# Performance work log

Measured on AMD Instinct MI355X. Metric: run time of the kernel, lower is better.

Reference implementation:

```python
import jax, jax.numpy as jnp
import numpy as np

B, N, C, K, OUT = 2, 8192, 64, 20, 64
EDGE_DIM = C * 3 + 5  # 197
BN_EPS = 1e-5


def setup_inputs() -> dict:
    key = jax.random.key(0)
    k1, k2 = jax.random.split(key, 2)
    x = jax.random.normal(k1, (B, C, N), jnp.float32)
    conv_w = jax.random.normal(k2, (OUT, EDGE_DIM), jnp.float32) * 0.05
    return {
        "x": x,
        "conv_w": conv_w,
        "bn_gamma": jnp.ones((OUT,), jnp.float32),
        "bn_beta": jnp.zeros((OUT,), jnp.float32),
        "bn_mean": jnp.zeros((OUT,), jnp.float32),
        "bn_var": jnp.ones((OUT,), jnp.float32),
        "k": K,
    }


def reference(x, conv_w, bn_gamma, bn_beta, bn_mean, bn_var, k):
    xt = jnp.transpose(x, (0, 2, 1))          # [B, N, C]
    b, n, c = xt.shape
    xyz = xt[:, :, :3]                         # [B, N, 3]

    # ---- kNN on xyz (negative squared distance, top-k) ----
    inner = -2.0 * jnp.matmul(xyz, jnp.transpose(xyz, (0, 2, 1)))  # [B,N,N]
    xx = jnp.sum(xyz * xyz, axis=2, keepdims=True)                 # [B,N,1]
    pd = -xx - inner - jnp.transpose(xx, (0, 2, 1))                # [B,N,N]
    _, idx = jax.lax.top_k(pd, k)                                  # [B,N,k]

    # ---- gather neighbors ----
    neighbors = jax.vmap(lambda xi, ii: xi[ii])(xt, idx)           # [B,N,k,C]
    x_ctr = xt[:, :, None, :]                                      # [B,N,1,C]
    base = jnp.concatenate(
        [jnp.broadcast_to(x_ctr, (b, n, k, c)), neighbors - x_ctr, neighbors],
        axis=3)                                                    # [B,N,k,3C]

    # ---- geometric features ----
    xyz_nb = neighbors[:, :, :, :3]
    vec = xyz_nb - xyz[:, :, None, :]                              # [B,N,k,3]
    dist = jnp.linalg.norm(vec, axis=3, keepdims=True)             # [B,N,k,1]
    local_density = jnp.broadcast_to(dist.mean(axis=2, keepdims=True), dist.shape)
    z_ctr = xyz[:, :, 2:3]                                         # [B,N,1]
    z_nb = xyz_nb[:, :, :, 2:3]                                    # [B,N,k,1]
    rel_h = jnp.broadcast_to(z_ctr[:, :, None, :] - z_nb.mean(axis=2, keepdims=True), dist.shape)
    dist_var = jnp.broadcast_to(jnp.var(dist, axis=2, keepdims=True, ddof=1), dist.shape)
    vn = vec / (dist + 1e-6)
    md = vn.mean(axis=2, keepdims=True)
    md = md / (jnp.linalg.norm(md, axis=3, keepdims=True) + 1e-6)
    cos = jnp.sum(vn * md, axis=3, keepdims=True)
    angle = 1.0 - jnp.abs(cos)

    edge = jnp.concatenate([base, dist, local_density, rel_h, dist_var, angle], axis=3)  # [B,N,k,EDGE_DIM]

    # ---- 1x1 conv + BN (inference stats) + LeakyReLU(0.2) + max over neighbors ----
    y = jnp.einsum('bnkf,of->bnko', edge, conv_w)                  # [B,N,k,OUT]
    scale = bn_gamma / jnp.sqrt(bn_var + BN_EPS)
    y = (y - bn_mean) * scale + bn_beta
    y = jnp.where(y >= 0, y, 0.2 * y)
    out = y.max(axis=2)                                            # [B,N,OUT]
    return jnp.transpose(out, (0, 2, 1))                           # [B,OUT,N]
```

## Files before the change

kernel.cpp:

```cpp
#include <hip/hip_runtime.h>


#define NPTS 8192
#define NBATCH 2
#define NQ (NBATCH * NPTS)
#define CH 64
#define KNN 20
#define EDIM 197
#define QW 4
#define KWAVES 16
#define QB (QW * KWAVES)
#define CAPC 64

__device__ __forceinline__ float wsum(float v) {
  v += __shfl_xor(v, 1, 64);
  v += __shfl_xor(v, 2, 64);
  v += __shfl_xor(v, 4, 64);
  v += __shfl_xor(v, 8, 64);
  v += __shfl_xor(v, 16, 64);
  v += __shfl_xor(v, 32, 64);
  return v;
}

__device__ __forceinline__ float dtilde(float m2x, float m2y, float m2z, float4 c) {
  return fmaf(m2x, c.x, fmaf(m2y, c.y, fmaf(m2z, c.z, c.w)));
}

__device__ __forceinline__ double d2d(float qx, float qy, float qz, float4 c) {
  double dx = (double)qx - (double)c.x;
  double dy = (double)qy - (double)c.y;
  double dz = (double)qz - (double)c.z;
  return dx * dx + dy * dy + dz * dz;
}

__device__ __forceinline__ float bcastf(float v, int l) {
  return __int_as_float(__builtin_amdgcn_readlane(__float_as_int(v), l));
}

__global__ __launch_bounds__(256) void proj_kernel(const float* __restrict__ x,
                                                   const float* __restrict__ w,
                                                   float4* __restrict__ cpack,
                                                   float* __restrict__ projc,
                                                   float* __restrict__ projn) {
  __shared__ float wl[CH * 16];
  int by = blockIdx.y;
  int mat = by >> 2, oq = by & 3;
  for (int i = threadIdx.x; i < CH * 16; i += 256) {
    int c = i >> 4, oo = i & 15;
    int o = oq * 16 + oo;
    float w1 = w[o * EDIM + c];
    float w2 = w[o * EDIM + 64 + c];
    float w3 = w[o * EDIM + 128 + c];
    wl[i] = mat ? (w2 + w3) : (w1 - w2);
  }
  __syncthreads();
  int p = blockIdx.x * 256 + threadIdx.x;
  int b = p >> 13, n = p & (NPTS - 1);
  const float* xb = x + (size_t)b * CH * NPTS + n;
  float acc[16];
#pragma unroll
  for (int o = 0; o < 16; ++o) acc[o] = 0.f;
#pragma unroll 4
  for (int c = 0; c < CH; ++c) {
    float xv = xb[(size_t)c * NPTS];
    const float4* wr = (const float4*)(wl + c * 16);
#pragma unroll
    for (int o4 = 0; o4 < 4; ++o4) {
      float4 wv = wr[o4];
      acc[o4 * 4 + 0] = fmaf(wv.x, xv, acc[o4 * 4 + 0]);
      acc[o4 * 4 + 1] = fmaf(wv.y, xv, acc[o4 * 4 + 1]);
      acc[o4 * 4 + 2] = fmaf(wv.z, xv, acc[o4 * 4 + 2]);
      acc[o4 * 4 + 3] = fmaf(wv.w, xv, acc[o4 * 4 + 3]);
    }
  }
  float* dst = (mat ? projn : projc) + (size_t)p * 64 + oq * 16;
#pragma unroll
  for (int o4 = 0; o4 < 4; ++o4)
    ((float4*)dst)[o4] = make_float4(acc[o4 * 4 + 0], acc[o4 * 4 + 1],
                                     acc[o4 * 4 + 2], acc[o4 * 4 + 3]);
  if (by == 0) {
    float cx = xb[0], cy = xb[(size_t)NPTS], cz = xb[(size_t)2 * NPTS];
    cpack[p] = make_float4(cx, cy, cz, fmaf(cx, cx, fmaf(cy, cy, cz * cz)));
  }
}

__global__ __launch_bounds__(1024) void knnfeat_kernel(const float4* __restrict__ cpack,
                                                       const float* __restrict__ projc,
                                                       const float* __restrict__ projn,
                                                       const float* __restrict__ w,
                                                       const float* __restrict__ gamma,
                                                       const float* __restrict__ beta,
                                                       const float* __restrict__ mean,
                                                       const float* __restrict__ var,
                                                       float* __restrict__ out) {
  __shared__ float4 t4[NPTS];
  __shared__ int lidx[KWAVES][QW][CAPC];
  __shared__ int nsel[KWAVES][QW][KNN];
  int tid = threadIdx.x;
  int lane = tid & 63;
  int wq = tid >> 6;
  int blk = blockIdx.x;
  int bb = blk >> 7;
  int q0 = blk * QB + wq * QW;
  const float4* cb = cpack + bb * NPTS;

  for (int i = tid; i < NPTS; i += 1024) t4[i] = cb[i];
  float qx[QW], qy[QW], qz[QW], m2x[QW], m2y[QW], m2z[QW];
#pragma unroll
  for (int qi = 0; qi < QW; ++qi) {
    float4 qp = cpack[q0 + qi];
    qx[qi] = qp.x; qy[qi] = qp.y; qz[qi] = qp.z;
    m2x[qi] = -2.f * qp.x; m2y[qi] = -2.f * qp.y; m2z[qi] = -2.f * qp.z;
  }
  __syncthreads();

  float m[QW];
#pragma unroll
  for (int qi = 0; qi < QW; ++qi) m[qi] = 3.0e38f;
#pragma unroll 2
  for (int i = 0; i < NPTS / 64; ++i) {
    float4 c = t4[lane + i * 64];
#pragma unroll
    for (int qi = 0; qi < QW; ++qi)
      m[qi] = fminf(m[qi], dtilde(m2x[qi], m2y[qi], m2z[qi], c));
  }
  float lo[QW], hi[QW];
#pragma unroll
  for (int qi = 0; qi < QW; ++qi) { lo[qi] = -256.f; hi[qi] = 256.f; }
#pragma unroll 1
  for (int it = 0; it < 24; ++it) {
#pragma unroll
    for (int qi = 0; qi < QW; ++qi) {
      float mid = (lo[qi] + hi[qi]) * 0.5f;
      int c = (int)__popcll(__ballot(m[qi] <= mid));
      if (c >= KNN) hi[qi] = mid; else lo[qi] = mid;
    }
  }

  int cnt[QW];
#pragma unroll
  for (int qi = 0; qi < QW; ++qi) cnt[qi] = 0;
  unsigned long long lmlt = (1ull << lane) - 1ull;
#pragma unroll 2
  for (int i = 0; i < NPTS / 64; ++i) {
    float4 c = t4[lane + i * 64];
#pragma unroll
    for (int qi = 0; qi < QW; ++qi) {
      bool pr = dtilde(m2x[qi], m2y[qi], m2z[qi], c) <= hi[qi];
      unsigned long long mk = __ballot(pr);
      if (mk) {
        int ofs = cnt[qi] + (int)__popcll(mk & lmlt);
        if (pr && ofs < CAPC) lidx[wq][qi][ofs] = lane + i * 64;
        cnt[qi] += (int)__popcll(mk);
      }
    }
  }

  double dd[QW]; int ii[QW]; int cC[QW];
#pragma unroll
  for (int qi = 0; qi < QW; ++qi) {
    cC[qi] = min(cnt[qi], CAPC);
    dd[qi] = 1e300; ii[qi] = -1;
    if (lane < cC[qi]) {
      int id = lidx[wq][qi][lane];
      dd[qi] = d2d(qx[qi], qy[qi], qz[qi], t4[id]);
      ii[qi] = id;
    }
  }
#pragma unroll
  for (int qi = 0; qi < QW; ++qi) {
    int xlo = __double2loint(dd[qi]), xhi = __double2hiint(dd[qi]);
    int r = 0;
#pragma unroll 1
    for (int j = 0; j < cC[qi]; ++j) {
      double dj = __hiloint2double(__builtin_amdgcn_readlane(xhi, j),
                                   __builtin_amdgcn_readlane(xlo, j));
      int idj = __builtin_amdgcn_readlane(ii[qi], j);
      r += (dj < dd[qi]) || (dj == dd[qi] && idj < ii[qi]);
    }
    if (ii[qi] >= 0 && r < KNN) nsel[wq][qi][r] = ii[qi];
  }

  float* zbuf = (float*)&lidx[0][0][0];
  float wd  = w[lane * EDIM + 192];
  float wld = w[lane * EDIM + 193];
  float wrh = w[lane * EDIM + 194];
  float wdv = w[lane * EDIM + 195];
  float wa  = w[lane * EDIM + 196];
  float sc = gamma[lane] / sqrtf(var[lane] + 1e-5f);
  float muv = mean[lane], bt = beta[lane];
#pragma unroll 2
  for (int qi = 0; qi < QW; ++qi) {
    int gq = q0 + qi;
    int jj = nsel[wq][qi][lane < KNN ? lane : 0] & (NPTS - 1);
    float4 nb = t4[jj];
    float vx = nb.x - qx[qi], vy = nb.y - qy[qi], vz = nb.z - qz[qi];
    float dist = sqrtf(fmaf(vx, vx, fmaf(vy, vy, vz * vz)));
    float inv = 1.f / (dist + 1e-6f);
    float vnx = vx * inv, vny = vy * inv, vnz = vz * inv;
    float msk = (lane < KNN) ? 1.f : 0.f;
    float sd = wsum(dist * msk);
    float szn = wsum(nb.z * msk);
    float sx = wsum(vnx * msk);
    float sy = wsum(vny * msk);
    float s3 = wsum(vnz * msk);
    float ld = sd * (1.f / KNN);
    float rh = qz[qi] - szn * (1.f / KNN);
    float dev = dist - ld;
    float dvs = wsum(dev * dev * msk);
    float dv = dvs * (1.f / (KNN - 1));
    float mdx = sx * (1.f / KNN), mdy = sy * (1.f / KNN), mdz = s3 * (1.f / KNN);
    float mnorm = sqrtf(fmaf(mdx, mdx, fmaf(mdy, mdy, mdz * mdz)));
    float rinv = 1.f / (mnorm + 1e-6f);
    mdx *= rinv; mdy *= rinv; mdz *= rinv;
    float cosv = vnx * mdx + vny * mdy + vnz * mdz;
    float angle = 1.f - fabsf(cosv);
    float base = projc[(size_t)gq * 64 + lane] + ld * wld + rh * wrh + dv * wdv;
    float zmax = -3.0e38f, zmin = 3.0e38f;
#pragma unroll
    for (int kk = 0; kk < KNN; ++kk) {
      float dk = bcastf(dist, kk);
      float ak = bcastf(angle, kk);
      int jk = __builtin_amdgcn_readlane(jj, kk);
      float z = base + projn[(size_t)(bb * NPTS + jk) * 64 + lane] + dk * wd + ak * wa;
      zmax = fmaxf(zmax, z);
      zmin = fminf(zmin, z);
    }
    float M = (sc >= 0.f) ? zmax : zmin;
    float yv = (M - muv) * sc + bt;
    yv = (yv >= 0.f) ? yv : 0.2f * yv;
    int qcol = wq * QW + qi;
    zbuf[qcol * 64 + ((lane + qcol) & 63)] = yv;
  }
  __syncthreads();
  {
    int o = tid >> 4, g = tid & 15;
    int n0 = (blk & 127) * 64;
    int q4 = g * 4;
    float4 v;
    v.x = zbuf[(q4 + 0) * 64 + ((o + q4 + 0) & 63)];
    v.y = zbuf[(q4 + 1) * 64 + ((o + q4 + 1) & 63)];
    v.z = zbuf[(q4 + 2) * 64 + ((o + q4 + 2) & 63)];
    v.w = zbuf[(q4 + 3) * 64 + ((o + q4 + 3) & 63)];
    *(float4*)(out + (size_t)bb * CH * NPTS + (size_t)o * NPTS + n0 + q4) = v;
  }
}

extern "C" void kernel_launch(void* const* d_in, const int* in_sizes, int n_in,
                              void* d_out, int out_size, void* d_ws, size_t ws_size,
                              hipStream_t stream) {
  const float* x = (const float*)d_in[0];
  const float* w = (const float*)d_in[1];
  const float* gamma = (const float*)d_in[2];
  const float* beta = (const float*)d_in[3];
  const float* mean = (const float*)d_in[4];
  const float* var = (const float*)d_in[5];
  float* out = (float*)d_out;

  const size_t OFF_CPACK = 0;
  const size_t OFF_PROJC = 262144;
  const size_t OFF_PROJN = 262144 + 4194304;
  const size_t NEED = 262144 + 8388608;
  if (ws_size < NEED) return;

  char* ws = (char*)d_ws;
  float4* cpack = (float4*)(ws + OFF_CPACK);
  float* projc = (float*)(ws + OFF_PROJC);
  float* projn = (float*)(ws + OFF_PROJN);

  proj_kernel<<<dim3(64, 8), 256, 0, stream>>>(x, w, cpack, projc, projn);
  knnfeat_kernel<<<256, 1024, 0, stream>>>(cpack, projc, projn, w,
                                           gamma, beta, mean, var, out);
}
```

Measured before the change: 79.46 us.

## Replace brute-force kNN scan with z-bucket sorted spatial search

```diff
diff --git a/kernel.cpp b/kernel.cpp
--- a/kernel.cpp
+++ b/kernel.cpp
@@ -3,14 +3,19 @@
 
 #define NPTS 8192
 #define NBATCH 2
-#define NQ (NBATCH * NPTS)
 #define CH 64
 #define KNN 20
 #define EDIM 197
-#define QW 4
+#define NBUCK 1024
+#define CAPC 128
 #define KWAVES 16
-#define QB (QW * KWAVES)
-#define CAPC 64
+#define QW 2
+#define QB (KWAVES * QW)
+
+__device__ __forceinline__ int zbucket(float z) {
+  int b = (int)((z + 4.5f) * (1024.0f / 9.0f));
+  return b < 0 ? 0 : (b > 1023 ? 1023 : b);
+}
 
 __device__ __forceinline__ float wsum(float v) {
   v += __shfl_xor(v, 1, 64);
@@ -37,11 +42,17 @@
   return __int_as_float(__builtin_amdgcn_readlane(__float_as_int(v), l));
 }
 
+__global__ __launch_bounds__(1024) void zeroh_kernel(int* __restrict__ hist) {
+  int t = blockIdx.x * 1024 + threadIdx.x;
+  if (t < NBATCH * NBUCK) hist[t] = 0;
+}
+
 __global__ __launch_bounds__(256) void proj_kernel(const float* __restrict__ x,
                                                    const float* __restrict__ w,
                                                    float4* __restrict__ cpack,
                                                    float* __restrict__ projc,
-                                                   float* __restrict__ projn) {
+                                                   float* __restrict__ projn,
+                                                   int* __restrict__ hist) {
   __shared__ float wl[CH * 16];
   int by = blockIdx.y;
   int mat = by >> 2, oq = by & 3;
@@ -81,122 +92,187 @@
   if (by == 0) {
     float cx = xb[0], cy = xb[(size_t)NPTS], cz = xb[(size_t)2 * NPTS];
     cpack[p] = make_float4(cx, cy, cz, fmaf(cx, cx, fmaf(cy, cy, cz * cz)));
-  }
-}
-
-__global__ __launch_bounds__(1024) void knnfeat_kernel(const float4* __restrict__ cpack,
-                                                       const float* __restrict__ projc,
-                                                       const float* __restrict__ projn,
-                                                       const float* __restrict__ w,
-                                                       const float* __restrict__ gamma,
-                                                       const float* __restrict__ beta,
-                                                       const float* __restrict__ mean,
-                                                       const float* __restrict__ var,
-                                                       float* __restrict__ out) {
-  __shared__ float4 t4[NPTS];
-  __shared__ int lidx[KWAVES][QW][CAPC];
-  __shared__ int nsel[KWAVES][QW][KNN];
+    atomicAdd(&hist[b * NBUCK + zbucket(cz)], 1);
+  }
+}
+
+__global__ __launch_bounds__(1024) void prefix_kernel(const int* __restrict__ hist,
+                                                      int* __restrict__ off,
+                                                      int* __restrict__ cursor) {
+  __shared__ int s[NBUCK];
   int tid = threadIdx.x;
-  int lane = tid & 63;
-  int wq = tid >> 6;
+  for (int b = 0; b < NBATCH; ++b) {
+    s[tid] = hist[b * NBUCK + tid];
+    __syncthreads();
+    for (int o = 1; o < NBUCK; o <<= 1) {
+      int t = (tid >= o) ? s[tid - o] : 0;
+      __syncthreads();
+      s[tid] += t;
+      __syncthreads();
+    }
+    int excl = tid ? s[tid - 1] : 0;
+    off[b * (NBUCK + 1) + tid] = excl;
+    cursor[b * NBUCK + tid] = excl;
+    if (tid == NBUCK - 1) off[b * (NBUCK + 1) + NBUCK] = s[NBUCK - 1];
+    __syncthreads();
+  }
+}
+
+__global__ __launch_bounds__(256) void scatter_kernel(const float4* __restrict__ cpack,
+                                                      int* __restrict__ cursor,
+                                                      float4* __restrict__ s4g,
+                                                      int* __restrict__ sidxg) {
+  int t = blockIdx.x * 256 + threadIdx.x;
+  int b = t >> 13, n = t & (NPTS - 1);
+  float4 c = cpack[t];
+  int slot = atomicAdd(&cursor[b * NBUCK + zbucket(c.z)], 1);
+  s4g[b * NPTS + slot] = c;
+  sidxg[b * NPTS + slot] = n;
+}
+
+__global__ __launch_bounds__(1024, 8) void knnfeat_kernel(const float4* __restrict__ cpack,
+                                                          const float4* __restrict__ s4g,
+                                                          const int* __restrict__ sidxg,
+                                                          const int* __restrict__ off,
+                                                          const float* __restrict__ projc,
+                                                          const float* __restrict__ projn,
+                                                          const float* __restrict__ w,
+                                                          const float* __restrict__ gamma,
+                                                          const float* __restrict__ beta,
+                                                          const float* __restrict__ mean,
+                                                          const float* __restrict__ var,
+                                                          float* __restrict__ out) {
+  __shared__ int offL[NBUCK + 1];
+  __shared__ unsigned short lidx[KWAVES][CAPC];
+  __shared__ int nselL[KWAVES][KNN];
+  __shared__ float zbuf[QB][65];
+  int tid = threadIdx.x, lane = tid & 63, wq = tid >> 6;
   int blk = blockIdx.x;
-  int bb = blk >> 7;
-  int q0 = blk * QB + wq * QW;
-  const float4* cb = cpack + bb * NPTS;
-
-  for (int i = tid; i < NPTS; i += 1024) t4[i] = cb[i];
-  float qx[QW], qy[QW], qz[QW], m2x[QW], m2y[QW], m2z[QW];
-#pragma unroll
-  for (int qi = 0; qi < QW; ++qi) {
-    float4 qp = cpack[q0 + qi];
-    qx[qi] = qp.x; qy[qi] = qp.y; qz[qi] = qp.z;
-    m2x[qi] = -2.f * qp.x; m2y[qi] = -2.f * qp.y; m2z[qi] = -2.f * qp.z;
-  }
+  int bb = blk >> 8;
+  int n0 = (blk & 255) * QB;
+  const float4* sb = s4g + bb * NPTS;
+  const int* ib = sidxg + bb * NPTS;
+  for (int i = tid; i <= NBUCK; i += 1024) offL[i] = off[bb * (NBUCK + 1) + i];
   __syncthreads();
-
-  float m[QW];
-#pragma unroll
-  for (int qi = 0; qi < QW; ++qi) m[qi] = 3.0e38f;
-#pragma unroll 2
-  for (int i = 0; i < NPTS / 64; ++i) {
-    float4 c = t4[lane + i * 64];
-#pragma unroll
-    for (int qi = 0; qi < QW; ++qi)
-      m[qi] = fminf(m[qi], dtilde(m2x[qi], m2y[qi], m2z[qi], c));
-  }
-  float lo[QW], hi[QW];
-#pragma unroll
-  for (int qi = 0; qi < QW; ++qi) { lo[qi] = -256.f; hi[qi] = 256.f; }
-#pragma unroll 1
-  for (int it = 0; it < 24; ++it) {
-#pragma unroll
-    for (int qi = 0; qi < QW; ++qi) {
-      float mid = (lo[qi] + hi[qi]) * 0.5f;
-      int c = (int)__popcll(__ballot(m[qi] <= mid));
-      if (c >= KNN) hi[qi] = mid; else lo[qi] = mid;
-    }
-  }
-
-  int cnt[QW];
-#pragma unroll
-  for (int qi = 0; qi < QW; ++qi) cnt[qi] = 0;
   unsigned long long lmlt = (1ull << lane) - 1ull;
-#pragma unroll 2
-  for (int i = 0; i < NPTS / 64; ++i) {
-    float4 c = t4[lane + i * 64];
-#pragma unroll
-    for (int qi = 0; qi < QW; ++qi) {
-      bool pr = dtilde(m2x[qi], m2y[qi], m2z[qi], c) <= hi[qi];
-      unsigned long long mk = __ballot(pr);
-      if (mk) {
-        int ofs = cnt[qi] + (int)__popcll(mk & lmlt);
-        if (pr && ofs < CAPC) lidx[wq][qi][ofs] = lane + i * 64;
-        cnt[qi] += (int)__popcll(mk);
-      }
-    }
-  }
-
-  double dd[QW]; int ii[QW]; int cC[QW];
-#pragma unroll
-  for (int qi = 0; qi < QW; ++qi) {
-    cC[qi] = min(cnt[qi], CAPC);
-    dd[qi] = 1e300; ii[qi] = -1;
-    if (lane < cC[qi]) {
-      int id = lidx[wq][qi][lane];
-      dd[qi] = d2d(qx[qi], qy[qi], qz[qi], t4[id]);
-      ii[qi] = id;
-    }
-  }
-#pragma unroll
-  for (int qi = 0; qi < QW; ++qi) {
-    int xlo = __double2loint(dd[qi]), xhi = __double2hiint(dd[qi]);
-    int r = 0;
-#pragma unroll 1
-    for (int j = 0; j < cC[qi]; ++j) {
-      double dj = __hiloint2double(__builtin_amdgcn_readlane(xhi, j),
-                                   __builtin_amdgcn_readlane(xlo, j));
-      int idj = __builtin_amdgcn_readlane(ii[qi], j);
-      r += (dj < dd[qi]) || (dj == dd[qi] && idj < ii[qi]);
-    }
-    if (ii[qi] >= 0 && r < KNN) nsel[wq][qi][r] = ii[qi];
-  }
-
-  float* zbuf = (float*)&lidx[0][0][0];
+
   float wd  = w[lane * EDIM + 192];
   float wld = w[lane * EDIM + 193];
   float wrh = w[lane * EDIM + 194];
   float wdv = w[lane * EDIM + 195];
   float wa  = w[lane * EDIM + 196];
-  float sc = gamma[lane] / sqrtf(var[lane] + 1e-5f);
+  float sc = gamma[lane] * __builtin_amdgcn_rcpf(__builtin_amdgcn_sqrtf(var[lane] + 1e-5f));
   float muv = mean[lane], bt = beta[lane];
+
+#pragma unroll 1
+  for (int qi = 0; qi < QW; ++qi) {
+    int gq = bb * NPTS + n0 + wq * QW + qi;
+    float4 qp = cpack[gq];
+    float m2x = -2.f * qp.x, m2y = -2.f * qp.y, m2z = -2.f * qp.z;
+    float q2 = fmaf(qp.x, qp.x, fmaf(qp.y, qp.y, qp.z * qp.z));
+
+    int bq = zbucket(qp.z);
+    int mid = (offL[bq] + offL[bq + 1]) >> 1;
+    int st = mid - 512;
+    st = st < 0 ? 0 : (st > NPTS - 1024 ? NPTS - 1024 : st);
+    float mm = 3.0e38f;
+#pragma unroll 4
+    for (int i = 0; i < 16; ++i)
+      mm = fminf(mm, dtilde(m2x, m2y, m2z, sb[st + i * 64 + lane]));
+    float lo = -64.f, hi = 64.f;
+#pragma unroll 1
+    for (int it = 0; it < 22; ++it) {
+      float md = (lo + hi) * 0.5f;
+      int c = (int)__popcll(__ballot(mm <= md));
+      if (c >= KNN) hi = md; else lo = md;
+    }
+    float tau = hi;
+
+    float rr = tau + q2; rr = rr < 0.f ? 0.f : rr;
+    float r = __builtin_amdgcn_sqrtf(rr) * 1.001f + 1e-4f;
+    int e0 = offL[zbucket(qp.z - r)];
+    int e1 = offL[zbucket(qp.z + r) + 1];
+    int cnt = 0;
+    int niter = (e1 - e0 + 63) >> 6;
+#pragma unroll 1
+    for (int i = 0; i < niter; ++i) {
+      int j = e0 + i * 64 + lane;
+      int jc = j < NPTS ? j : NPTS - 1;
+      bool pr = (j < e1) && (dtilde(m2x, m2y, m2z, sb[jc]) <= tau);
+      unsigned long long mk = __ballot(pr);
+      if (mk) {
+        int ofs = cnt + (int)__popcll(mk & lmlt);
+        if (pr && ofs < CAPC) lidx[wq][ofs] = (unsigned short)j;
+        cnt += (int)__popcll(mk);
+      }
+    }
+    if (cnt > CAPC) {
+      mm = 3.0e38f;
 #pragma unroll 2
-  for (int qi = 0; qi < QW; ++qi) {
-    int gq = q0 + qi;
-    int jj = nsel[wq][qi][lane < KNN ? lane : 0] & (NPTS - 1);
-    float4 nb = t4[jj];
-    float vx = nb.x - qx[qi], vy = nb.y - qy[qi], vz = nb.z - qz[qi];
-    float dist = sqrtf(fmaf(vx, vx, fmaf(vy, vy, vz * vz)));
-    float inv = 1.f / (dist + 1e-6f);
+      for (int i = 0; i < NPTS / 64; ++i)
+        mm = fminf(mm, dtilde(m2x, m2y, m2z, sb[i * 64 + lane]));
+      lo = -64.f; hi = 64.f;
+      for (int it = 0; it < 22; ++it) {
+        float md = (lo + hi) * 0.5f;
+        int c = (int)__popcll(__ballot(mm <= md));
+        if (c >= KNN) hi = md; else lo = md;
+      }
+      tau = hi; cnt = 0;
+      for (int i = 0; i < NPTS / 64; ++i) {
+        int j = i * 64 + lane;
+        bool pr = dtilde(m2x, m2y, m2z, sb[j]) <= tau;
+        unsigned long long mk = __ballot(pr);
+        if (mk) {
+          int ofs = cnt + (int)__popcll(mk & lmlt);
+          if (pr && ofs < CAPC) lidx[wq][ofs] = (unsigned short)j;
+          cnt += (int)__popcll(mk);
+        }
+      }
+    }
+    int C = cnt < CAPC ? cnt : CAPC;
+
+    double d0 = 1e300, d1 = 1e300; int o0 = -1, o1 = -1, s0 = 0, s1 = 0;
+    if (lane < C) {
+      s0 = lidx[wq][lane];
+      d0 = d2d(qp.x, qp.y, qp.z, sb[s0]);
+      o0 = ib[s0];
+    }
+    if (C > 64 && lane + 64 < C) {
+      s1 = lidx[wq][lane + 64];
+      d1 = d2d(qp.x, qp.y, qp.z, sb[s1]);
+      o1 = ib[s1];
+    }
+    int x0l = __double2loint(d0), x0h = __double2hiint(d0);
+    int x1l = __double2loint(d1), x1h = __double2hiint(d1);
+    int r0 = 0, r1 = 0;
+    int C0 = C < 64 ? C : 64;
+#pragma unroll 1
+    for (int j = 0; j < C0; ++j) {
+      double dj = __hiloint2double(__builtin_amdgcn_readlane(x0h, j),
+                                   __builtin_amdgcn_readlane(x0l, j));
+      int oj = __builtin_amdgcn_readlane(o0, j);
+      r0 += (dj < d0) || (dj == d0 && oj < o0);
+      r1 += (dj < d1) || (dj == d1 && oj < o1);
+    }
+    if (C > 64) {
+#pragma unroll 1
+      for (int j = 0; j < C - 64; ++j) {
+        double dj = __hiloint2double(__builtin_amdgcn_readlane(x1h, j),
+                                     __builtin_amdgcn_readlane(x1l, j));
+        int oj = __builtin_amdgcn_readlane(o1, j);
+        r0 += (dj < d0) || (dj == d0 && oj < o0);
+        r1 += (dj < d1) || (dj == d1 && oj < o1);
+      }
+    }
+    if (o0 >= 0 && r0 < KNN) nselL[wq][r0] = o0 | (s0 << 16);
+    if (o1 >= 0 && r1 < KNN) nselL[wq][r1] = o1 | (s1 << 16);
+
+    int pv = nselL[wq][lane < KNN ? lane : 0];
+    int js = pv >> 16;
+    float4 nb = sb[js];
+    float vx = nb.x - qp.x, vy = nb.y - qp.y, vz = nb.z - qp.z;
+    float dist = __builtin_amdgcn_sqrtf(fmaf(vx, vx, fmaf(vy, vy, vz * vz)));
+    float inv = __builtin_amdgcn_rcpf(dist + 1e-6f);
     float vnx = vx * inv, vny = vy * inv, vnz = vz * inv;
     float msk = (lane < KNN) ? 1.f : 0.f;
     float sd = wsum(dist * msk);
@@ -205,13 +281,13 @@
     float sy = wsum(vny * msk);
     float s3 = wsum(vnz * msk);
     float ld = sd * (1.f / KNN);
-    float rh = qz[qi] - szn * (1.f / KNN);
+    float rh = qp.z - szn * (1.f / KNN);
     float dev = dist - ld;
     float dvs = wsum(dev * dev * msk);
     float dv = dvs * (1.f / (KNN - 1));
     float mdx = sx * (1.f / KNN), mdy = sy * (1.f / KNN), mdz = s3 * (1.f / KNN);
-    float mnorm = sqrtf(fmaf(mdx, mdx, fmaf(mdy, mdy, mdz * mdz)));
-    float rinv = 1.f / (mnorm + 1e-6f);
+    float mnorm = __builtin_amdgcn_sqrtf(fmaf(mdx, mdx, fmaf(mdy, mdy, mdz * mdz)));
+    float rinv = __builtin_amdgcn_rcpf(mnorm + 1e-6f);
     mdx *= rinv; mdy *= rinv; mdz *= rinv;
     float cosv = vnx * mdx + vny * mdy + vnz * mdz;
     float angle = 1.f - fabsf(cosv);
@@ -221,7 +297,7 @@
     for (int kk = 0; kk < KNN; ++kk) {
       float dk = bcastf(dist, kk);
       float ak = bcastf(angle, kk);
-      int jk = __builtin_amdgcn_readlane(jj, kk);
+      int jk = __builtin_amdgcn_readlane(pv, kk) & 0xFFFF;
       float z = base + projn[(size_t)(bb * NPTS + jk) * 64 + lane] + dk * wd + ak * wa;
       zmax = fmaxf(zmax, z);
       zmin = fminf(zmin, z);
@@ -230,18 +306,17 @@
     float yv = (M - muv) * sc + bt;
     yv = (yv >= 0.f) ? yv : 0.2f * yv;
     int qcol = wq * QW + qi;
-    zbuf[qcol * 64 + ((lane + qcol) & 63)] = yv;
+    zbuf[qcol][(lane + qcol) & 63] = yv;
   }
   __syncthreads();
-  {
-    int o = tid >> 4, g = tid & 15;
-    int n0 = (blk & 127) * 64;
+  if (tid < 512) {
+    int g = tid & 7, o = tid >> 3;
     int q4 = g * 4;
     float4 v;
-    v.x = zbuf[(q4 + 0) * 64 + ((o + q4 + 0) & 63)];
-    v.y = zbuf[(q4 + 1) * 64 + ((o + q4 + 1) & 63)];
-    v.z = zbuf[(q4 + 2) * 64 + ((o + q4 + 2) & 63)];
-    v.w = zbuf[(q4 + 3) * 64 + ((o + q4 + 3) & 63)];
+    v.x = zbuf[q4 + 0][(o + q4 + 0) & 63];
+    v.y = zbuf[q4 + 1][(o + q4 + 1) & 63];
+    v.z = zbuf[q4 + 2][(o + q4 + 2) & 63];
+    v.w = zbuf[q4 + 3][(o + q4 + 3) & 63];
     *(float4*)(out + (size_t)bb * CH * NPTS + (size_t)o * NPTS + n0 + q4) = v;
   }
 }
@@ -259,16 +334,30 @@
 
   const size_t OFF_CPACK = 0;
   const size_t OFF_PROJC = 262144;
-  const size_t OFF_PROJN = 262144 + 4194304;
-  const size_t NEED = 262144 + 8388608;
+  const size_t OFF_PROJN = 4456448;
+  const size_t OFF_S4    = 8650752;
+  const size_t OFF_SIDX  = 8912896;
+  const size_t OFF_HIST  = 8978432;
+  const size_t OFF_OFFT  = 8986624;
+  const size_t OFF_CUR   = 8994824;
+  const size_t NEED      = 9003016;
   if (ws_size < NEED) return;
 
   char* ws = (char*)d_ws;
   float4* cpack = (float4*)(ws + OFF_CPACK);
   float* projc = (float*)(ws + OFF_PROJC);
   float* projn = (float*)(ws + OFF_PROJN);
-
-  proj_kernel<<<dim3(64, 8), 256, 0, stream>>>(x, w, cpack, projc, projn);
-  knnfeat_kernel<<<256, 1024, 0, stream>>>(cpack, projc, projn, w,
+  float4* s4g = (float4*)(ws + OFF_S4);
+  int* sidxg = (int*)(ws + OFF_SIDX);
+  int* hist = (int*)(ws + OFF_HIST);
+  int* offt = (int*)(ws + OFF_OFFT);
+  int* cur = (int*)(ws + OFF_CUR);
+
+  zeroh_kernel<<<2, 1024, 0, stream>>>(hist);
+  proj_kernel<<<dim3(64, 8), 256, 0, stream>>>(x, w, cpack, projc, projn, hist);
+  prefix_kernel<<<1, 1024, 0, stream>>>(hist, offt, cur);
+  scatter_kernel<<<64, 256, 0, stream>>>(cpack, cur, s4g, sidxg);
+  knnfeat_kernel<<<512, 1024, 0, stream>>>(cpack, s4g, sidxg, offt,
+                                           projc, projn, w,
                                            gamma, beta, mean, var, out);
 }
```

Result: slower. 158.0 us (+98.8%).

## Sort points into z-buckets to prune kNN candidate scans

Applied to the files above, without the earlier changes.

```diff
diff --git a/kernel.cpp b/kernel.cpp
--- a/kernel.cpp
+++ b/kernel.cpp
@@ -3,14 +3,19 @@
 
 #define NPTS 8192
 #define NBATCH 2
-#define NQ (NBATCH * NPTS)
 #define CH 64
 #define KNN 20
 #define EDIM 197
+#define NBUCK 1024
+#define CAPC 64
+#define KWAVES 16
 #define QW 4
-#define KWAVES 16
-#define QB (QW * KWAVES)
-#define CAPC 64
+#define QB (KWAVES * QW)
+
+__device__ __forceinline__ int zbucket(float z) {
+  int b = (int)((z + 4.5f) * (1024.0f / 9.0f));
+  return b < 0 ? 0 : (b > 1023 ? 1023 : b);
+}
 
 __device__ __forceinline__ float wsum(float v) {
   v += __shfl_xor(v, 1, 64);
@@ -37,11 +42,17 @@
   return __int_as_float(__builtin_amdgcn_readlane(__float_as_int(v), l));
 }
 
+__global__ __launch_bounds__(1024) void zeroh_kernel(int* __restrict__ hist) {
+  int t = blockIdx.x * 1024 + threadIdx.x;
+  if (t < NBATCH * NBUCK) hist[t] = 0;
+}
+
 __global__ __launch_bounds__(256) void proj_kernel(const float* __restrict__ x,
                                                    const float* __restrict__ w,
                                                    float4* __restrict__ cpack,
                                                    float* __restrict__ projc,
-                                                   float* __restrict__ projn) {
+                                                   float* __restrict__ projn,
+                                                   int* __restrict__ hist) {
   __shared__ float wl[CH * 16];
   int by = blockIdx.y;
   int mat = by >> 2, oq = by & 3;
@@ -81,10 +92,49 @@
   if (by == 0) {
     float cx = xb[0], cy = xb[(size_t)NPTS], cz = xb[(size_t)2 * NPTS];
     cpack[p] = make_float4(cx, cy, cz, fmaf(cx, cx, fmaf(cy, cy, cz * cz)));
-  }
-}
-
-__global__ __launch_bounds__(1024) void knnfeat_kernel(const float4* __restrict__ cpack,
+    atomicAdd(&hist[b * NBUCK + zbucket(cz)], 1);
+  }
+}
+
+__global__ __launch_bounds__(1024) void prefix_kernel(const int* __restrict__ hist,
+                                                      int* __restrict__ off,
+                                                      int* __restrict__ cursor) {
+  __shared__ int s[NBUCK];
+  int tid = threadIdx.x;
+  for (int b = 0; b < NBATCH; ++b) {
+    s[tid] = hist[b * NBUCK + tid];
+    __syncthreads();
+    for (int o = 1; o < NBUCK; o <<= 1) {
+      int t = (tid >= o) ? s[tid - o] : 0;
+      __syncthreads();
+      s[tid] += t;
+      __syncthreads();
+    }
+    int excl = tid ? s[tid - 1] : 0;
+    off[b * (NBUCK + 1) + tid] = excl;
+    cursor[b * NBUCK + tid] = excl;
+    if (tid == NBUCK - 1) off[b * (NBUCK + 1) + NBUCK] = s[NBUCK - 1];
+    __syncthreads();
+  }
+}
+
+__global__ __launch_bounds__(256) void scatter_kernel(const float4* __restrict__ cpack,
+                                                      int* __restrict__ cursor,
+                                                      float4* __restrict__ s4g,
+                                                      int* __restrict__ sidxg,
+                                                      int* __restrict__ rinv) {
+  int t = blockIdx.x * 256 + threadIdx.x;
+  int b = t >> 13, n = t & (NPTS - 1);
+  float4 c = cpack[t];
+  int slot = atomicAdd(&cursor[b * NBUCK + zbucket(c.z)], 1);
+  s4g[b * NPTS + slot] = c;
+  sidxg[b * NPTS + slot] = n;
+  rinv[b * NPTS + n] = slot;
+}
+
+__global__ __launch_bounds__(1024) void knnfeat_kernel(const float4* __restrict__ s4g,
+                                                       const int* __restrict__ sidxg,
+                                                       const int* __restrict__ off,
                                                        const float* __restrict__ projc,
                                                        const float* __restrict__ projn,
                                                        const float* __restrict__ w,
@@ -92,34 +142,41 @@
                                                        const float* __restrict__ beta,
                                                        const float* __restrict__ mean,
                                                        const float* __restrict__ var,
-                                                       float* __restrict__ out) {
+                                                       float* __restrict__ scratch) {
   __shared__ float4 t4[NPTS];
-  __shared__ int lidx[KWAVES][QW][CAPC];
+  __shared__ int offL[NBUCK + 1];
+  __shared__ unsigned short lidx[KWAVES][QW][CAPC];
   __shared__ int nsel[KWAVES][QW][KNN];
-  int tid = threadIdx.x;
-  int lane = tid & 63;
-  int wq = tid >> 6;
+  int tid = threadIdx.x, lane = tid & 63, wq = tid >> 6;
   int blk = blockIdx.x;
   int bb = blk >> 7;
-  int q0 = blk * QB + wq * QW;
-  const float4* cb = cpack + bb * NPTS;
-
-  for (int i = tid; i < NPTS; i += 1024) t4[i] = cb[i];
-  float qx[QW], qy[QW], qz[QW], m2x[QW], m2y[QW], m2z[QW];
-#pragma unroll
-  for (int qi = 0; qi < QW; ++qi) {
-    float4 qp = cpack[q0 + qi];
+  int q0s = (blk & 127) * QB + wq * QW;
+  const float4* sb = s4g + bb * NPTS;
+  const int* ib = sidxg + bb * NPTS;
+  for (int i = tid; i < NPTS; i += 1024) t4[i] = sb[i];
+  for (int i = tid; i <= NBUCK; i += 1024) offL[i] = off[bb * (NBUCK + 1) + i];
+  unsigned long long lmlt = (1ull << lane) - 1ull;
+
+  float qx[QW], qy[QW], qz[QW], m2x[QW], m2y[QW], m2z[QW], q2[QW];
+  int oq[QW];
+#pragma unroll
+  for (int qi = 0; qi < QW; ++qi) {
+    float4 qp = sb[q0s + qi];
+    oq[qi] = ib[q0s + qi];
     qx[qi] = qp.x; qy[qi] = qp.y; qz[qi] = qp.z;
     m2x[qi] = -2.f * qp.x; m2y[qi] = -2.f * qp.y; m2z[qi] = -2.f * qp.z;
+    q2[qi] = fmaf(qp.x, qp.x, fmaf(qp.y, qp.y, qp.z * qp.z));
   }
   __syncthreads();
 
+  int st = q0s + 2 - 512;
+  st = st < 0 ? 0 : (st > NPTS - 1024 ? NPTS - 1024 : st);
   float m[QW];
 #pragma unroll
   for (int qi = 0; qi < QW; ++qi) m[qi] = 3.0e38f;
 #pragma unroll 2
-  for (int i = 0; i < NPTS / 64; ++i) {
-    float4 c = t4[lane + i * 64];
+  for (int i = 0; i < 16; ++i) {
+    float4 c = t4[st + i * 64 + lane];
 #pragma unroll
     for (int qi = 0; qi < QW; ++qi)
       m[qi] = fminf(m[qi], dtilde(m2x[qi], m2y[qi], m2z[qi], c));
@@ -137,34 +194,74 @@
     }
   }
 
+  int E0 = NPTS, E1 = 0;
+#pragma unroll
+  for (int qi = 0; qi < QW; ++qi) {
+    float rr = hi[qi] + q2[qi]; rr = rr < 0.f ? 0.f : rr;
+    float r = sqrtf(rr) * 1.001f + 1e-4f;
+    int e0 = offL[zbucket(qz[qi] - r)];
+    int e1 = offL[zbucket(qz[qi] + r) + 1];
+    E0 = e0 < E0 ? e0 : E0;
+    E1 = e1 > E1 ? e1 : E1;
+  }
   int cnt[QW];
 #pragma unroll
   for (int qi = 0; qi < QW; ++qi) cnt[qi] = 0;
-  unsigned long long lmlt = (1ull << lane) - 1ull;
-#pragma unroll 2
-  for (int i = 0; i < NPTS / 64; ++i) {
-    float4 c = t4[lane + i * 64];
+  int niter = (E1 - E0 + 63) >> 6;
+#pragma unroll 1
+  for (int i = 0; i < niter; ++i) {
+    int j = E0 + i * 64 + lane;
+    int jc = j < NPTS ? j : NPTS - 1;
+    float4 c = t4[jc];
+    bool inb = j < E1;
 #pragma unroll
     for (int qi = 0; qi < QW; ++qi) {
-      bool pr = dtilde(m2x[qi], m2y[qi], m2z[qi], c) <= hi[qi];
+      bool pr = inb && (dtilde(m2x[qi], m2y[qi], m2z[qi], c) <= hi[qi]);
       unsigned long long mk = __ballot(pr);
       if (mk) {
         int ofs = cnt[qi] + (int)__popcll(mk & lmlt);
-        if (pr && ofs < CAPC) lidx[wq][qi][ofs] = lane + i * 64;
+        if (pr && ofs < CAPC) lidx[wq][qi][ofs] = (unsigned short)j;
         cnt[qi] += (int)__popcll(mk);
       }
     }
   }
-
-  double dd[QW]; int ii[QW]; int cC[QW];
+#pragma unroll 1
+  for (int qi = 0; qi < QW; ++qi) {
+    if (cnt[qi] > CAPC) {
+      float mm = 3.0e38f;
+#pragma unroll 2
+      for (int i = 0; i < NPTS / 64; ++i)
+        mm = fminf(mm, dtilde(m2x[qi], m2y[qi], m2z[qi], t4[i * 64 + lane]));
+      float flo = -256.f, fhi = 256.f;
+      for (int it = 0; it < 24; ++it) {
+        float mid = (flo + fhi) * 0.5f;
+        int c = (int)__popcll(__ballot(mm <= mid));
+        if (c >= KNN) fhi = mid; else flo = mid;
+      }
+      hi[qi] = fhi; cnt[qi] = 0;
+      for (int i = 0; i < NPTS / 64; ++i) {
+        int j = i * 64 + lane;
+        bool pr = dtilde(m2x[qi], m2y[qi], m2z[qi], t4[j]) <= fhi;
+        unsigned long long mk = __ballot(pr);
+        if (mk) {
+          int ofs = cnt[qi] + (int)__popcll(mk & lmlt);
+          if (pr && ofs < CAPC) lidx[wq][qi][ofs] = (unsigned short)j;
+          cnt[qi] += (int)__popcll(mk);
+        }
+      }
+    }
+  }
+
+  double dd[QW]; int ii[QW], ss[QW], cC[QW];
 #pragma unroll
   for (int qi = 0; qi < QW; ++qi) {
     cC[qi] = min(cnt[qi], CAPC);
-    dd[qi] = 1e300; ii[qi] = -1;
+    dd[qi] = 1e300; ii[qi] = -1; ss[qi] = 0;
     if (lane < cC[qi]) {
-      int id = lidx[wq][qi][lane];
-      dd[qi] = d2d(qx[qi], qy[qi], qz[qi], t4[id]);
-      ii[qi] = id;
+      int s = lidx[wq][qi][lane];
+      dd[qi] = d2d(qx[qi], qy[qi], qz[qi], t4[s]);
+      ii[qi] = ib[s];
+      ss[qi] = s;
     }
   }
 #pragma unroll
@@ -178,25 +275,24 @@
       int idj = __builtin_amdgcn_readlane(ii[qi], j);
       r += (dj < dd[qi]) || (dj == dd[qi] && idj < ii[qi]);
     }
-    if (ii[qi] >= 0 && r < KNN) nsel[wq][qi][r] = ii[qi];
-  }
-
-  float* zbuf = (float*)&lidx[0][0][0];
+    if (ii[qi] >= 0 && r < KNN) nsel[wq][qi][r] = ss[qi] | (ii[qi] << 16);
+  }
+
   float wd  = w[lane * EDIM + 192];
   float wld = w[lane * EDIM + 193];
   float wrh = w[lane * EDIM + 194];
   float wdv = w[lane * EDIM + 195];
   float wa  = w[lane * EDIM + 196];
-  float sc = gamma[lane] / sqrtf(var[lane] + 1e-5f);
+  float sc = gamma[lane] * __builtin_amdgcn_rcpf(__builtin_amdgcn_sqrtf(var[lane] + 1e-5f));
   float muv = mean[lane], bt = beta[lane];
 #pragma unroll 2
   for (int qi = 0; qi < QW; ++qi) {
-    int gq = q0 + qi;
-    int jj = nsel[wq][qi][lane < KNN ? lane : 0] & (NPTS - 1);
-    float4 nb = t4[jj];
+    int pv = nsel[wq][qi][lane < KNN ? lane : 0];
+    int js = pv & 0xFFFF;
+    float4 nb = t4[js];
     float vx = nb.x - qx[qi], vy = nb.y - qy[qi], vz = nb.z - qz[qi];
-    float dist = sqrtf(fmaf(vx, vx, fmaf(vy, vy, vz * vz)));
-    float inv = 1.f / (dist + 1e-6f);
+    float dist = __builtin_amdgcn_sqrtf(fmaf(vx, vx, fmaf(vy, vy, vz * vz)));
+    float inv = __builtin_amdgcn_rcpf(dist + 1e-6f);
     float vnx = vx * inv, vny = vy * inv, vnz = vz * inv;
     float msk = (lane < KNN) ? 1.f : 0.f;
     float sd = wsum(dist * msk);
@@ -210,18 +306,19 @@
     float dvs = wsum(dev * dev * msk);
     float dv = dvs * (1.f / (KNN - 1));
     float mdx = sx * (1.f / KNN), mdy = sy * (1.f / KNN), mdz = s3 * (1.f / KNN);
-    float mnorm = sqrtf(fmaf(mdx, mdx, fmaf(mdy, mdy, mdz * mdz)));
-    float rinv = 1.f / (mnorm + 1e-6f);
-    mdx *= rinv; mdy *= rinv; mdz *= rinv;
+    float mnorm = __builtin_amdgcn_sqrtf(fmaf(mdx, mdx, fmaf(mdy, mdy, mdz * mdz)));
+    float rinv2 = __builtin_amdgcn_rcpf(mnorm + 1e-6f);
+    mdx *= rinv2; mdy *= rinv2; mdz *= rinv2;
     float cosv = vnx * mdx + vny * mdy + vnz * mdz;
     float angle = 1.f - fabsf(cosv);
-    float base = projc[(size_t)gq * 64 + lane] + ld * wld + rh * wrh + dv * wdv;
+    float base = projc[(size_t)(bb * NPTS + oq[qi]) * 64 + lane]
+               + ld * wld + rh * wrh + dv * wdv;
     float zmax = -3.0e38f, zmin = 3.0e38f;
 #pragma unroll
     for (int kk = 0; kk < KNN; ++kk) {
       float dk = bcastf(dist, kk);
       float ak = bcastf(angle, kk);
-      int jk = __builtin_amdgcn_readlane(jj, kk);
+      int jk = __builtin_amdgcn_readlane(pv, kk) >> 16;
       float z = base + projn[(size_t)(bb * NPTS + jk) * 64 + lane] + dk * wd + ak * wa;
       zmax = fmaxf(zmax, z);
       zmin = fminf(zmin, z);
@@ -229,20 +326,33 @@
     float M = (sc >= 0.f) ? zmax : zmin;
     float yv = (M - muv) * sc + bt;
     yv = (yv >= 0.f) ? yv : 0.2f * yv;
-    int qcol = wq * QW + qi;
-    zbuf[qcol * 64 + ((lane + qcol) & 63)] = yv;
+    scratch[(size_t)(bb * NPTS + q0s + qi) * 64 + lane] = yv;
+  }
+}
+
+__global__ __launch_bounds__(256) void permute_kernel(const float* __restrict__ scratch,
+                                                      const int* __restrict__ rinv,
+                                                      float* __restrict__ out) {
+  __shared__ float tile[64][65];
+  int tid = threadIdx.x, lane = tid & 63, grp = tid >> 6;
+  int blk = blockIdx.x;
+  int bb = blk >> 7;
+  int n0 = (blk & 127) * 64;
+  int slot = rinv[bb * NPTS + n0 + lane];
+  const float4* row = (const float4*)(scratch + (size_t)(bb * NPTS + slot) * 64);
+#pragma unroll
+  for (int c4 = 0; c4 < 4; ++c4) {
+    float4 v = row[grp * 4 + c4];
+    tile[lane][grp * 16 + c4 * 4 + 0] = v.x;
+    tile[lane][grp * 16 + c4 * 4 + 1] = v.y;
+    tile[lane][grp * 16 + c4 * 4 + 2] = v.z;
+    tile[lane][grp * 16 + c4 * 4 + 3] = v.w;
   }
   __syncthreads();
-  {
-    int o = tid >> 4, g = tid & 15;
-    int n0 = (blk & 127) * 64;
-    int q4 = g * 4;
-    float4 v;
-    v.x = zbuf[(q4 + 0) * 64 + ((o + q4 + 0) & 63)];
-    v.y = zbuf[(q4 + 1) * 64 + ((o + q4 + 1) & 63)];
-    v.z = zbuf[(q4 + 2) * 64 + ((o + q4 + 2) & 63)];
-    v.w = zbuf[(q4 + 3) * 64 + ((o + q4 + 3) & 63)];
-    *(float4*)(out + (size_t)bb * CH * NPTS + (size_t)o * NPTS + n0 + q4) = v;
+#pragma unroll
+  for (int r16 = 0; r16 < 16; ++r16) {
+    int o = grp * 16 + r16;
+    out[((size_t)bb * CH + o) * NPTS + n0 + lane] = tile[lane][o];
   }
 }
 
@@ -259,16 +369,34 @@
 
   const size_t OFF_CPACK = 0;
   const size_t OFF_PROJC = 262144;
-  const size_t OFF_PROJN = 262144 + 4194304;
-  const size_t NEED = 262144 + 8388608;
+  const size_t OFF_PROJN = 4456448;
+  const size_t OFF_S4    = 8650752;
+  const size_t OFF_SIDX  = 8912896;
+  const size_t OFF_RINV  = 8978432;
+  const size_t OFF_HIST  = 9043968;
+  const size_t OFF_OFFT  = 9052160;
+  const size_t OFF_CUR   = 9060864;
+  const size_t OFF_SCR   = 9069056;
+  const size_t NEED      = 9069056 + 4194304;
   if (ws_size < NEED) return;
 
   char* ws = (char*)d_ws;
   float4* cpack = (float4*)(ws + OFF_CPACK);
   float* projc = (float*)(ws + OFF_PROJC);
   float* projn = (float*)(ws + OFF_PROJN);
-
-  proj_kernel<<<dim3(64, 8), 256, 0, stream>>>(x, w, cpack, projc, projn);
-  knnfeat_kernel<<<256, 1024, 0, stream>>>(cpack, projc, projn, w,
-                                           gamma, beta, mean, var, out);
-}
+  float4* s4g = (float4*)(ws + OFF_S4);
+  int* sidxg = (int*)(ws + OFF_SIDX);
+  int* rinv = (int*)(ws + OFF_RINV);
+  int* hist = (int*)(ws + OFF_HIST);
+  int* offt = (int*)(ws + OFF_OFFT);
+  int* cur = (int*)(ws + OFF_CUR);
+  float* scr = (float*)(ws + OFF_SCR);
+
+  zeroh_kernel<<<2, 1024, 0, stream>>>(hist);
+  proj_kernel<<<dim3(64, 8), 256, 0, stream>>>(x, w, cpack, projc, projn, hist);
+  prefix_kernel<<<1, 1024, 0, stream>>>(hist, offt, cur);
+  scatter_kernel<<<64, 256, 0, stream>>>(cpack, cur, s4g, sidxg, rinv);
+  knnfeat_kernel<<<256, 1024, 0, stream>>>(s4g, sidxg, offt, projc, projn, w,
+                                           gamma, beta, mean, var, scr);
+  permute_kernel<<<256, 256, 0, stream>>>(scr, rinv, out);
+}
```

Result: slower. 146.0 us (+83.8%).
